# Kernel tuning notes

Hardware: AMD Instinct MI355X
Metric: run time of the kernel (lower is better)

## Reference

```python
import jax, jax.numpy as jnp
import numpy as np

B, S, D, H = 2, 2048, 1024, 16
HS = D // H  # head size 64
EPS = 1e-5


def setup_inputs() -> dict:
    key = jax.random.key(0)
    ks = jax.random.split(key, 12)
    s = lambda fan_in: 1.0 / np.sqrt(fan_in)
    return {
        "x": jax.random.normal(ks[0], (B, S, D), dtype=jnp.float32),
        # per-head QKV weights, math orientation [H, D, HS] (x @ W)
        "wq": jax.random.normal(ks[1], (H, D, HS), dtype=jnp.float32) * s(D),
        "wk": jax.random.normal(ks[2], (H, D, HS), dtype=jnp.float32) * s(D),
        "wv": jax.random.normal(ks[3], (H, D, HS), dtype=jnp.float32) * s(D),
        "wproj": jax.random.normal(ks[4], (D, D), dtype=jnp.float32) * s(D),
        "bproj": jnp.zeros((D,), dtype=jnp.float32),
        "w1": jax.random.normal(ks[5], (D, 4 * D), dtype=jnp.float32) * s(D),
        "b1": jnp.zeros((4 * D,), dtype=jnp.float32),
        "w2": jax.random.normal(ks[6], (4 * D, D), dtype=jnp.float32) * s(4 * D),
        "b2": jnp.zeros((D,), dtype=jnp.float32),
        "ln1_g": jnp.ones((D,), dtype=jnp.float32),
        "ln1_b": jnp.zeros((D,), dtype=jnp.float32),
        "ln2_g": jnp.ones((D,), dtype=jnp.float32),
        "ln2_b": jnp.zeros((D,), dtype=jnp.float32),
    }


def _layernorm(x, g, b):
    mu = jnp.mean(x, axis=-1, keepdims=True)
    var = jnp.mean(jnp.square(x - mu), axis=-1, keepdims=True)
    return (x - mu) * jax.lax.rsqrt(var + EPS) * g + b


def reference(x, wq, wk, wv, wproj, bproj, w1, b1, w2, b2, ln1_g, ln1_b, ln2_g, ln2_b):
    Bq, T, C = x.shape
    xn = _layernorm(x, ln1_g, ln1_b)
    # per-head projections, batched over heads
    q = jnp.einsum('btd,hdk->bhtk', xn, wq)
    k = jnp.einsum('btd,hdk->bhtk', xn, wk)
    v = jnp.einsum('btd,hdk->bhtk', xn, wv)
    scale = k.shape[-1] ** (-0.5)
    scores = jnp.einsum('bhtk,bhsk->bhts', q, k) * scale  # [B,H,T,T]
    causal = jnp.tril(jnp.ones((T, T), dtype=bool))
    scores = jnp.where(causal, scores, -jnp.inf)
    att = jax.nn.softmax(scores, axis=-1)
    out = jnp.einsum('bhts,bhsk->bhtk', att, v)  # [B,H,T,HS]
    out = out.transpose(0, 2, 1, 3).reshape(Bq, T, C)  # concat heads
    attn_out = out @ wproj + bproj
    h = x + attn_out
    hn = _layernorm(h, ln2_g, ln2_b)
    ff = jax.nn.relu(hn @ w1 + b1) @ w2 + b2
    return h + ff
```

## Files before the change

kernel.cpp:

```cpp
#include <hip/hip_runtime.h>


typedef __bf16 bf16_t;
typedef __attribute__((ext_vector_type(8))) __bf16 bf16x8;
typedef __attribute__((ext_vector_type(4))) __bf16 bf16x4;
typedef __attribute__((ext_vector_type(4))) float f32x4;

__device__ __forceinline__ f32x4 mfma16(bf16x8 a, bf16x8 b, f32x4 c) {
  return __builtin_amdgcn_mfma_f32_16x16x32_bf16(a, b, c, 0, 0, 0);
}

__device__ __forceinline__ void gll16(const void* g, void* l) {
  __builtin_amdgcn_global_load_lds(
      (const __attribute__((address_space(1))) void*)g,
      (__attribute__((address_space(3))) void*)l, 16, 0, 0);
}

__global__ __launch_bounds__(256) void ln_kernel(
    const float* __restrict__ x, const float* __restrict__ g,
    const float* __restrict__ be, bf16_t* __restrict__ out) {
  const int row = blockIdx.x;
  const int tid = threadIdx.x;
  const float4 v = *(reinterpret_cast<const float4*>(x + (size_t)row * 1024) + tid);
  float s1 = v.x + v.y + v.z + v.w;
  float s2 = v.x * v.x + v.y * v.y + v.z * v.z + v.w * v.w;
#pragma unroll
  for (int off = 1; off < 64; off <<= 1) {
    s1 += __shfl_xor(s1, off);
    s2 += __shfl_xor(s2, off);
  }
  __shared__ float red[8];
  const int l = tid & 63, w = tid >> 6;
  if (l == 0) { red[w] = s1; red[w + 4] = s2; }
  __syncthreads();
  s1 = red[0] + red[1] + red[2] + red[3];
  s2 = red[4] + red[5] + red[6] + red[7];
  const float mu = s1 * (1.f / 1024.f);
  const float var = s2 * (1.f / 1024.f) - mu * mu;
  const float rstd = rsqrtf(var + 1e-5f);
  const float4 gg = *(reinterpret_cast<const float4*>(g) + tid);
  const float4 bb = *(reinterpret_cast<const float4*>(be) + tid);
  bf16x4 o;
  o[0] = (bf16_t)((v.x - mu) * rstd * gg.x + bb.x);
  o[1] = (bf16_t)((v.y - mu) * rstd * gg.y + bb.y);
  o[2] = (bf16_t)((v.z - mu) * rstd * gg.z + bb.z);
  o[3] = (bf16_t)((v.w - mu) * rstd * gg.w + bb.w);
  *(reinterpret_cast<bf16x4*>(out + (size_t)row * 1024) + tid) = o;
}

__global__ __launch_bounds__(256) void transpose_cvt(
    const float* __restrict__ in, bf16_t* __restrict__ out, int R, int C) {
  __shared__ float t[32][33];
  const int bz = blockIdx.z;
  in += (size_t)bz * R * C;
  out += (size_t)bz * R * C;
  const int c0 = blockIdx.x * 32, r0 = blockIdx.y * 32;
  const int tx = threadIdx.x, ty = threadIdx.y;
#pragma unroll
  for (int i = 0; i < 4; i++)
    t[ty + i * 8][tx] = in[(size_t)(r0 + ty + i * 8) * C + c0 + tx];
  __syncthreads();
#pragma unroll
  for (int i = 0; i < 4; i++)
    out[(size_t)(c0 + ty + i * 8) * R + r0 + tx] = (bf16_t)t[tx][ty + i * 8];
}

template <int MODE>
__global__ __launch_bounds__(256) void gemm_bt(
    const bf16_t* __restrict__ A, const bf16_t* __restrict__ BT,
    const float* __restrict__ bias, const float* __restrict__ resid,
    void* __restrict__ out0, void* __restrict__ out1, int M, int N, int K) {
  __shared__ __align__(16) bf16_t Al[128 * 32];
  __shared__ __align__(16) bf16_t Bl[128 * 32];
  const int tid = threadIdx.x;
  const int l = tid & 63, w = tid >> 6;
  const int wr = w >> 1, wc = w & 1;
  const int lr = l & 15, lg = l >> 4;
  const int gx = gridDim.x;
  const int nwg = gx * gridDim.y;
  int flat = blockIdx.y * gx + blockIdx.x;
  flat = (flat & 7) * (nwg >> 3) + (flat >> 3);
  const int bm = (flat / gx) * 128, bn = (flat % gx) * 128;

  f32x4 acc[4][4];
#pragma unroll
  for (int i = 0; i < 4; i++)
#pragma unroll
    for (int j = 0; j < 4; j++) acc[i][j] = (f32x4)(0.f);

  const char* Ag = (const char*)(A + (size_t)bm * K);
  const char* Bg = (const char*)(BT + (size_t)bn * K);
  const size_t rowb = (size_t)K * 2;
  const int nK = K >> 5;

  for (int kt = 0; kt < nK; ++kt) {
#pragma unroll
    for (int i = 0; i < 2; i++) {
      const int s = i * 256 + tid;
      const size_t go = (size_t)(s >> 2) * rowb + (size_t)(kt * 64 + (s & 3) * 16);
      gll16(Ag + go, (char*)Al + (i * 256 + w * 64) * 16);
      gll16(Bg + go, (char*)Bl + (i * 256 + w * 64) * 16);
    }
    __syncthreads();
    bf16x8 af[4], bfr[4];
#pragma unroll
    for (int mi = 0; mi < 4; mi++)
      af[mi] = *reinterpret_cast<const bf16x8*>(Al + (wr * 64 + mi * 16 + lr) * 32 + lg * 8);
#pragma unroll
    for (int ni = 0; ni < 4; ni++)
      bfr[ni] = *reinterpret_cast<const bf16x8*>(Bl + (wc * 64 + ni * 16 + lr) * 32 + lg * 8);
#pragma unroll
    for (int mi = 0; mi < 4; mi++)
#pragma unroll
      for (int ni = 0; ni < 4; ni++)
        acc[mi][ni] = mfma16(af[mi], bfr[ni], acc[mi][ni]);
    __syncthreads();
  }

#pragma unroll
  for (int mi = 0; mi < 4; mi++) {
    const int r = bm + wr * 64 + mi * 16 + lg * 4;
#pragma unroll
    for (int ni = 0; ni < 4; ni++) {
      const int c = bn + wc * 64 + ni * 16 + lr;
      f32x4 v = acc[mi][ni];
      if constexpr (MODE == 1) {
        const float bb = bias[c];
        float* o = (float*)out0;
#pragma unroll
        for (int j = 0; j < 4; j++)
          o[(size_t)(r + j) * N + c] = v[j] + bb + resid[(size_t)(r + j) * N + c];
      } else if constexpr (MODE == 2) {
        const float bb = bias[c];
        bf16_t* o = (bf16_t*)out0;
#pragma unroll
        for (int j = 0; j < 4; j++)
          o[(size_t)(r + j) * N + c] = (bf16_t)fmaxf(v[j] + bb, 0.f);
      } else {
        if (c < 2048) {
          bf16_t* o = (bf16_t*)out0;
#pragma unroll
          for (int j = 0; j < 4; j++)
            o[(size_t)(r + j) * 2048 + c] = (bf16_t)v[j];
        } else {
          const int nn = c - 2048;
          const int bI = r >> 11, tl = r & 2047;
          bf16x4 pk;
#pragma unroll
          for (int j = 0; j < 4; j++) pk[j] = (bf16_t)v[j];
          *reinterpret_cast<bf16x4*>((bf16_t*)out1 +
              ((size_t)(bI * 1024 + nn)) * 2048 + tl) = pk;
        }
      }
    }
  }
}

__device__ __forceinline__ void attn_tile(
    const bf16_t* __restrict__ kl, const bf16_t* __restrict__ vl,
    bf16_t* __restrict__ plw, const bf16x8* qf, f32x4* oacc,
    float* mrow, float* lrow, const int lr, const int lg,
    const int rbase, const int cbase, const bool diag) {
  f32x4 sc4[4];
#pragma unroll
  for (int ct = 0; ct < 4; ct++) sc4[ct] = (f32x4)(0.f);
#pragma unroll
  for (int ct = 0; ct < 4; ct++)
#pragma unroll
    for (int kc = 0; kc < 2; kc++) {
      bf16x8 kf = *reinterpret_cast<const bf16x8*>(
          &kl[(ct * 16 + lr) * 72 + kc * 32 + lg * 8]);
      sc4[ct] = mfma16(qf[kc], kf, sc4[ct]);
    }
#pragma unroll
  for (int ct = 0; ct < 4; ct++)
#pragma unroll
    for (int j = 0; j < 4; j++) {
      float sv = sc4[ct][j] * 0.125f;
      if (diag && (cbase + ct * 16 + lr > rbase + j)) sv = -1e30f;
      sc4[ct][j] = sv;
    }
  float rmax[4];
#pragma unroll
  for (int j = 0; j < 4; j++)
    rmax[j] = fmaxf(fmaxf(sc4[0][j], sc4[1][j]), fmaxf(sc4[2][j], sc4[3][j]));
#pragma unroll
  for (int off = 1; off < 16; off <<= 1)
#pragma unroll
    for (int j = 0; j < 4; j++) rmax[j] = fmaxf(rmax[j], __shfl_xor(rmax[j], off));
  float fac[4];
#pragma unroll
  for (int j = 0; j < 4; j++) {
    const float mn = fmaxf(mrow[j], rmax[j]);
    fac[j] = __expf(mrow[j] - mn);
    mrow[j] = mn;
  }
  float rsum[4] = {0.f, 0.f, 0.f, 0.f};
#pragma unroll
  for (int ct = 0; ct < 4; ct++)
#pragma unroll
    for (int j = 0; j < 4; j++) {
      const float pv = __expf(sc4[ct][j] - mrow[j]);
      sc4[ct][j] = pv;
      rsum[j] += pv;
    }
#pragma unroll
  for (int off = 1; off < 16; off <<= 1)
#pragma unroll
    for (int j = 0; j < 4; j++) rsum[j] += __shfl_xor(rsum[j], off);
#pragma unroll
  for (int j = 0; j < 4; j++) lrow[j] = lrow[j] * fac[j] + rsum[j];
#pragma unroll
  for (int ht = 0; ht < 4; ht++)
#pragma unroll
    for (int j = 0; j < 4; j++) oacc[ht][j] *= fac[j];
#pragma unroll
  for (int ct = 0; ct < 4; ct++)
#pragma unroll
    for (int j = 0; j < 4; j++)
      plw[(lg * 4 + j) * 72 + ct * 16 + lr] = (bf16_t)sc4[ct][j];
  bf16x8 pf[2];
#pragma unroll
  for (int sc = 0; sc < 2; sc++)
    pf[sc] = *reinterpret_cast<const bf16x8*>(&plw[lr * 72 + sc * 32 + lg * 8]);
#pragma unroll
  for (int ht = 0; ht < 4; ht++)
#pragma unroll
    for (int sc = 0; sc < 2; sc++) {
      bf16x8 vf = *reinterpret_cast<const bf16x8*>(
          &vl[(ht * 16 + lr) * 72 + sc * 32 + lg * 8]);
      oacc[ht] = mfma16(pf[sc], vf, oacc[ht]);
    }
}

__global__ __launch_bounds__(256) void attn_kernel(
    const bf16_t* __restrict__ qk, const bf16_t* __restrict__ vT,
    bf16_t* __restrict__ ac) {
  const int f = blockIdx.x;
  const int bh = (f & 7) + 8 * ((f >> 3) & 3);
  const int p = f >> 5;
  const int qlo = p, qhi = 31 - p;
  const int b = bh >> 4, h = bh & 15;
  const int tid = threadIdx.x;
  const int l = tid & 63, w = tid >> 6;
  const int lr = l & 15, lg = l >> 4;

  __shared__ __align__(16) bf16_t kl[64 * 72];
  __shared__ __align__(16) bf16_t vl[64 * 72];
  __shared__ __align__(16) bf16_t pl[4][16 * 72];
  bf16_t* plw = pl[w];

  const bf16_t* qb = qk + ((size_t)(b * 2048 + w * 16 + lr)) * 2048 + h * 64;
  bf16x8 qfl[2], qfh[2];
#pragma unroll
  for (int kc = 0; kc < 2; kc++) {
    qfl[kc] = *(const bf16x8*)(qb + (size_t)qlo * 64 * 2048 + kc * 32 + lg * 8);
    qfh[kc] = *(const bf16x8*)(qb + (size_t)qhi * 64 * 2048 + kc * 32 + lg * 8);
  }

  f32x4 oaccl[4], oacch[4];
  float ml[4], llo[4], mh[4], lhi[4];
#pragma unroll
  for (int i = 0; i < 4; i++) { oaccl[i] = (f32x4)(0.f); oacch[i] = (f32x4)(0.f); }
#pragma unroll
  for (int j = 0; j < 4; j++) { ml[j] = -1e30f; llo[j] = 0.f; mh[j] = -1e30f; lhi[j] = 0.f; }

  const int rlo = qlo * 64 + w * 16 + lg * 4;
  const int rhi = qhi * 64 + w * 16 + lg * 4;

  const int r0 = tid >> 3, c0 = (tid & 7) * 8;
  const bf16_t* kg = qk + ((size_t)(b * 2048)) * 2048 + 1024 + h * 64;
  const bf16_t* vg = vT + ((size_t)(bh * 64)) * 2048;

  bf16x8 kreg[2], vreg[2];
#pragma unroll
  for (int i = 0; i < 2; i++) {
    const int r = r0 + i * 32;
    kreg[i] = *(const bf16x8*)(kg + (size_t)r * 2048 + c0);
    vreg[i] = *(const bf16x8*)(vg + (size_t)r * 2048 + c0);
  }

  const int nst = qhi + 1;
  for (int st = 0; st < nst; ++st) {
    __syncthreads();
#pragma unroll
    for (int i = 0; i < 2; i++) {
      const int r = r0 + i * 32;
      *(bf16x8*)(&kl[r * 72 + c0]) = kreg[i];
      *(bf16x8*)(&vl[r * 72 + c0]) = vreg[i];
    }
    __syncthreads();
    if (st + 1 < nst) {
#pragma unroll
      for (int i = 0; i < 2; i++) {
        const int r = r0 + i * 32;
        kreg[i] = *(const bf16x8*)(kg + (size_t)((st + 1) * 64 + r) * 2048 + c0);
        vreg[i] = *(const bf16x8*)(vg + (size_t)r * 2048 + (st + 1) * 64 + c0);
      }
    }
    attn_tile(kl, vl, plw, qfh, oacch, mh, lhi, lr, lg, rhi, st * 64, st == qhi);
    if (st <= qlo)
      attn_tile(kl, vl, plw, qfl, oaccl, ml, llo, lr, lg, rlo, st * 64, st == qlo);
  }

#pragma unroll
  for (int ht = 0; ht < 4; ht++)
#pragma unroll
    for (int j = 0; j < 4; j++) {
      const size_t tl = (size_t)(b * 2048 + rlo + j);
      ac[tl * 1024 + h * 64 + ht * 16 + lr] = (bf16_t)(oaccl[ht][j] / llo[j]);
      const size_t th = (size_t)(b * 2048 + rhi + j);
      ac[th * 1024 + h * 64 + ht * 16 + lr] = (bf16_t)(oacch[ht][j] / lhi[j]);
    }
}

extern "C" void kernel_launch(void* const* d_in, const int* in_sizes, int n_in,
                              void* d_out, int out_size, void* d_ws, size_t ws_size,
                              hipStream_t stream) {
  const float* x     = (const float*)d_in[0];
  const float* wq    = (const float*)d_in[1];
  const float* wk    = (const float*)d_in[2];
  const float* wv    = (const float*)d_in[3];
  const float* wproj = (const float*)d_in[4];
  const float* bproj = (const float*)d_in[5];
  const float* w1    = (const float*)d_in[6];
  const float* b1    = (const float*)d_in[7];
  const float* w2    = (const float*)d_in[8];
  const float* b2    = (const float*)d_in[9];
  const float* ln1g  = (const float*)d_in[10];
  const float* ln1b  = (const float*)d_in[11];
  const float* ln2g  = (const float*)d_in[12];
  const float* ln2b  = (const float*)d_in[13];
  float* out = (float*)d_out;

  char* ws = (char*)d_ws;
  const size_t MB = 1 << 20;
  bf16_t* xn  = (bf16_t*)(ws + 0);
  bf16_t* wT  = (bf16_t*)(ws + 8 * MB);
  float*  hbuf= (float*)(ws + 16 * MB);
  bf16_t* qkb = (bf16_t*)(ws + 32 * MB);
  bf16_t* vTb = (bf16_t*)(ws + 48 * MB);
  bf16_t* acb = (bf16_t*)(ws + 56 * MB);
  bf16_t* ffa = (bf16_t*)(ws + 32 * MB);
  bf16_t* hn  = xn;

  dim3 tb(32, 8);

  ln_kernel<<<4096, 256, 0, stream>>>(x, ln1g, ln1b, xn);
  transpose_cvt<<<dim3(2, 32, 16), tb, 0, stream>>>(wq, wT, 1024, 64);
  transpose_cvt<<<dim3(2, 32, 16), tb, 0, stream>>>(wk, wT + 1024 * 1024, 1024, 64);
  transpose_cvt<<<dim3(2, 32, 16), tb, 0, stream>>>(wv, wT + 2048 * 1024, 1024, 64);
  gemm_bt<0><<<dim3(24, 32), 256, 0, stream>>>(xn, wT, nullptr, nullptr, qkb, vTb,
                                               4096, 3072, 1024);
  attn_kernel<<<512, 256, 0, stream>>>(qkb, vTb, acb);
  transpose_cvt<<<dim3(32, 32, 1), tb, 0, stream>>>(wproj, wT, 1024, 1024);
  gemm_bt<1><<<dim3(8, 32), 256, 0, stream>>>(acb, wT, bproj, x, hbuf, nullptr,
                                              4096, 1024, 1024);
  ln_kernel<<<4096, 256, 0, stream>>>(hbuf, ln2g, ln2b, hn);
  transpose_cvt<<<dim3(128, 32, 1), tb, 0, stream>>>(w1, wT, 1024, 4096);
  gemm_bt<2><<<dim3(32, 32), 256, 0, stream>>>(hn, wT, b1, nullptr, ffa, nullptr,
                                               4096, 4096, 1024);
  transpose_cvt<<<dim3(32, 128, 1), tb, 0, stream>>>(w2, wT, 4096, 1024);
  gemm_bt<1><<<dim3(8, 32), 256, 0, stream>>>(ffa, wT, b2, hbuf, out, nullptr,
                                              4096, 1024, 4096);
}
```

Before: 425.9 us.

## Split-K the N=1024 GEMMs and fuse partial reduction with epilogue/LayerNorm

The projection and FFN2 GEMMs only launch 256 workgroups, which underfills the GPU. They now split K across 2 and 4 slices into fp32 partial buffers. New kernels sum the partials and apply bias and residual, and one of them also fuses the second LayerNorm. The gain in parallelism costs extra traffic to write and read the partials (16-64 MB), and the path only runs if the workspace is at least 128 MB.

```diff
diff --git a/kernel.cpp b/kernel.cpp
--- a/kernel.cpp
+++ b/kernel.cpp
@@ -48,6 +48,68 @@
   *(reinterpret_cast<bf16x4*>(out + (size_t)row * 1024) + tid) = o;
 }
 
+__global__ __launch_bounds__(256) void ln2_red_kernel(
+    const float* __restrict__ p, const float* __restrict__ bp,
+    const float* __restrict__ x, const float* __restrict__ g,
+    const float* __restrict__ be, float* __restrict__ hb,
+    bf16_t* __restrict__ out) {
+  const size_t PM = (size_t)4096 * 1024;
+  const int row = blockIdx.x;
+  const int tid = threadIdx.x;
+  const size_t ro = (size_t)row * 1024;
+  float4 v = *(reinterpret_cast<const float4*>(p + ro) + tid);
+  const float4 v1 = *(reinterpret_cast<const float4*>(p + PM + ro) + tid);
+  const float4 vb = *(reinterpret_cast<const float4*>(bp) + tid);
+  const float4 vx = *(reinterpret_cast<const float4*>(x + ro) + tid);
+  v.x += v1.x + vb.x + vx.x; v.y += v1.y + vb.y + vx.y;
+  v.z += v1.z + vb.z + vx.z; v.w += v1.w + vb.w + vx.w;
+  *(reinterpret_cast<float4*>(hb + ro) + tid) = v;
+  float s1 = v.x + v.y + v.z + v.w;
+  float s2 = v.x * v.x + v.y * v.y + v.z * v.z + v.w * v.w;
+#pragma unroll
+  for (int off = 1; off < 64; off <<= 1) {
+    s1 += __shfl_xor(s1, off);
+    s2 += __shfl_xor(s2, off);
+  }
+  __shared__ float red[8];
+  const int l = tid & 63, w = tid >> 6;
+  if (l == 0) { red[w] = s1; red[w + 4] = s2; }
+  __syncthreads();
+  s1 = red[0] + red[1] + red[2] + red[3];
+  s2 = red[4] + red[5] + red[6] + red[7];
+  const float mu = s1 * (1.f / 1024.f);
+  const float var = s2 * (1.f / 1024.f) - mu * mu;
+  const float rstd = rsqrtf(var + 1e-5f);
+  const float4 gg = *(reinterpret_cast<const float4*>(g) + tid);
+  const float4 bb = *(reinterpret_cast<const float4*>(be) + tid);
+  bf16x4 o;
+  o[0] = (bf16_t)((v.x - mu) * rstd * gg.x + bb.x);
+  o[1] = (bf16_t)((v.y - mu) * rstd * gg.y + bb.y);
+  o[2] = (bf16_t)((v.z - mu) * rstd * gg.z + bb.z);
+  o[3] = (bf16_t)((v.w - mu) * rstd * gg.w + bb.w);
+  *(reinterpret_cast<bf16x4*>(out + ro) + tid) = o;
+}
+
+__global__ __launch_bounds__(256) void red4_kernel(
+    const float* __restrict__ p, const float* __restrict__ b2,
+    const float* __restrict__ hb, float* __restrict__ out) {
+  const size_t PM = (size_t)4096 * 1024;
+  const int row = blockIdx.x;
+  const int tid = threadIdx.x;
+  const size_t ro = (size_t)row * 1024;
+  float4 v = *(reinterpret_cast<const float4*>(p + ro) + tid);
+#pragma unroll
+  for (int s = 1; s < 4; s++) {
+    const float4 vs = *(reinterpret_cast<const float4*>(p + s * PM + ro) + tid);
+    v.x += vs.x; v.y += vs.y; v.z += vs.z; v.w += vs.w;
+  }
+  const float4 vb = *(reinterpret_cast<const float4*>(b2) + tid);
+  const float4 vh = *(reinterpret_cast<const float4*>(hb + ro) + tid);
+  v.x += vb.x + vh.x; v.y += vb.y + vh.y;
+  v.z += vb.z + vh.z; v.w += vb.w + vh.w;
+  *(reinterpret_cast<float4*>(out + ro) + tid) = v;
+}
+
 __global__ __launch_bounds__(256) void transpose_cvt(
     const float* __restrict__ in, bf16_t* __restrict__ out, int R, int C) {
   __shared__ float t[32][33];
@@ -82,16 +144,22 @@
   flat = (flat & 7) * (nwg >> 3) + (flat >> 3);
   const int bm = (flat / gx) * 128, bn = (flat % gx) * 128;
 
+  int k0 = 0, nK = K >> 5;
+  if constexpr (MODE == 3) {
+    const int chunk = K / gridDim.z;
+    k0 = blockIdx.z * chunk;
+    nK = chunk >> 5;
+  }
+
   f32x4 acc[4][4];
 #pragma unroll
   for (int i = 0; i < 4; i++)
 #pragma unroll
     for (int j = 0; j < 4; j++) acc[i][j] = (f32x4)(0.f);
 
-  const char* Ag = (const char*)(A + (size_t)bm * K);
-  const char* Bg = (const char*)(BT + (size_t)bn * K);
+  const char* Ag = (const char*)(A + (size_t)bm * K + k0);
+  const char* Bg = (const char*)(BT + (size_t)bn * K + k0);
   const size_t rowb = (size_t)K * 2;
-  const int nK = K >> 5;
 
   for (int kt = 0; kt < nK; ++kt) {
 #pragma unroll
@@ -136,6 +204,11 @@
 #pragma unroll
         for (int j = 0; j < 4; j++)
           o[(size_t)(r + j) * N + c] = (bf16_t)fmaxf(v[j] + bb, 0.f);
+      } else if constexpr (MODE == 3) {
+        float* o = (float*)out0 + (size_t)blockIdx.z * M * N;
+#pragma unroll
+        for (int j = 0; j < 4; j++)
+          o[(size_t)(r + j) * N + c] = v[j];
       } else {
         if (c < 2048) {
           bf16_t* o = (bf16_t*)out0;
@@ -342,8 +415,10 @@
   bf16_t* vTb = (bf16_t*)(ws + 48 * MB);
   bf16_t* acb = (bf16_t*)(ws + 56 * MB);
   bf16_t* ffa = (bf16_t*)(ws + 32 * MB);
+  float*  part= (float*)(ws + 64 * MB);
   bf16_t* hn  = xn;
 
+  const bool big = ws_size >= 128 * MB;
   dim3 tb(32, 8);
 
   ln_kernel<<<4096, 256, 0, stream>>>(x, ln1g, ln1b, xn);
@@ -354,13 +429,25 @@
                                                4096, 3072, 1024);
   attn_kernel<<<512, 256, 0, stream>>>(qkb, vTb, acb);
   transpose_cvt<<<dim3(32, 32, 1), tb, 0, stream>>>(wproj, wT, 1024, 1024);
-  gemm_bt<1><<<dim3(8, 32), 256, 0, stream>>>(acb, wT, bproj, x, hbuf, nullptr,
-                                              4096, 1024, 1024);
-  ln_kernel<<<4096, 256, 0, stream>>>(hbuf, ln2g, ln2b, hn);
+  if (big) {
+    gemm_bt<3><<<dim3(8, 32, 2), 256, 0, stream>>>(acb, wT, nullptr, nullptr,
+                                                   part, nullptr, 4096, 1024, 1024);
+    ln2_red_kernel<<<4096, 256, 0, stream>>>(part, bproj, x, ln2g, ln2b, hbuf, hn);
+  } else {
+    gemm_bt<1><<<dim3(8, 32), 256, 0, stream>>>(acb, wT, bproj, x, hbuf, nullptr,
+                                                4096, 1024, 1024);
+    ln_kernel<<<4096, 256, 0, stream>>>(hbuf, ln2g, ln2b, hn);
+  }
   transpose_cvt<<<dim3(128, 32, 1), tb, 0, stream>>>(w1, wT, 1024, 4096);
   gemm_bt<2><<<dim3(32, 32), 256, 0, stream>>>(hn, wT, b1, nullptr, ffa, nullptr,
                                                4096, 4096, 1024);
   transpose_cvt<<<dim3(32, 128, 1), tb, 0, stream>>>(w2, wT, 4096, 1024);
-  gemm_bt<1><<<dim3(8, 32), 256, 0, stream>>>(ffa, wT, b2, hbuf, out, nullptr,
-                                              4096, 1024, 4096);
-}
+  if (big) {
+    gemm_bt<3><<<dim3(8, 32, 4), 256, 0, stream>>>(ffa, wT, nullptr, nullptr,
+                                                   part, nullptr, 4096, 1024, 4096);
+    red4_kernel<<<4096, 256, 0, stream>>>(part, b2, hbuf, out);
+  } else {
+    gemm_bt<1><<<dim3(8, 32), 256, 0, stream>>>(ffa, wT, b2, hbuf, out, nullptr,
+                                                4096, 1024, 4096);
+  }
+}
```

Measured after the change: 413.0 us. 3.0% less time.
